# Kernel tuning notes

Hardware: AMD Instinct MI355X
Metric: run time of the kernel (lower is better)

Reference implementation:

```python
import jax, jax.numpy as jnp
import numpy as np

N, LT, LV, D, H = 4, 1024, 1024, 1024, 16
HD = D // H
EPS = 1e-12


def layernorm(x, w, b):
    u = x.mean(-1, keepdims=True)
    s = ((x - u) ** 2).mean(-1, keepdims=True)
    return w * (x - u) / jnp.sqrt(s + EPS) + b


def attention(q_in, k_in, v_in, mask, qw, qb, kw, kb, vw, vb):
    # mask: (N, Lq_or_1, Lk) float in {0,1}; torch Linear is x @ W.T + b
    def heads(x, w, b):
        y = x @ w.T + b
        return y.reshape(y.shape[0], y.shape[1], H, HD).transpose(0, 2, 1, 3)  # (N,H,L,hd)
    q, k, v = heads(q_in, qw, qb), heads(k_in, kw, kb), heads(v_in, vw, vb)
    scores = jnp.einsum('bhqd,bhkd->bhqk', q, k) / np.sqrt(HD).astype(np.float32)
    scores = scores + (1.0 - mask[:, None]) * (-10000.0)
    probs = jax.nn.softmax(scores, axis=-1)  # dropout is identity in eval
    ctx = jnp.einsum('bhqk,bhkd->bhqd', probs, v)
    return ctx.transpose(0, 2, 1, 3).reshape(q_in.shape[0], q_in.shape[1], D)


def setup_inputs() -> dict:
    key = jax.random.key(0)
    ks = jax.random.split(key, 16)
    inp = {
        'dec_hidden_states': jax.random.normal(ks[0], (N, LT, D), jnp.float32),
        'enc_outputs': jax.random.normal(ks[1], (N, LV, D), jnp.float32),
        'dec_mask': jnp.ones((N, LT), jnp.float32),
        'enc_mask': jnp.ones((N, LV), jnp.float32),
    }
    wnames = ['sa_qw', 'sa_kw', 'sa_vw', 'ca_qw', 'ca_kw', 'ca_vw', 'out_w']
    for i, n in enumerate(wnames):
        inp[n] = jax.random.normal(ks[2 + i], (D, D), jnp.float32) * 0.02
    for n in ['sa_qb', 'sa_kb', 'sa_vb', 'ca_qb', 'ca_kb', 'ca_vb', 'out_b', 'n1_b', 'n2_b', 'out_ln_b']:
        inp[n] = jnp.zeros((D,), jnp.float32)
    for n in ['n1_w', 'n2_w', 'out_ln_w']:
        inp[n] = jnp.ones((D,), jnp.float32)
    return inp


def reference(dec_hidden_states, enc_outputs, dec_mask, enc_mask,
              sa_qw, sa_qb, sa_kw, sa_kb, sa_vw, sa_vb, n1_w, n1_b,
              ca_qw, ca_qb, ca_kw, ca_kb, ca_vw, ca_vb, n2_w, n2_b,
              out_w, out_b, out_ln_w, out_ln_b):
    Lt = dec_mask.shape[1]
    # diagonal_mask=True: causal tril combined with padding mask
    self_mask = dec_mask[:, None, :] * jnp.tril(jnp.ones((Lt, Lt), dec_mask.dtype))  # (N,Lt,Lt)
    a = attention(dec_hidden_states, dec_hidden_states, dec_hidden_states, self_mask,
                  sa_qw, sa_qb, sa_kw, sa_kb, sa_vw, sa_vb)
    a = layernorm(a + dec_hidden_states, n1_w, n1_b)
    c = attention(a, enc_outputs, enc_outputs, enc_mask[:, None, :],
                  ca_qw, ca_qb, ca_kw, ca_kb, ca_vw, ca_vb)
    c = layernorm(a + c, n2_w, n2_b)
    # BertOutput called as output(x, x): dense, residual, LN (dropout = identity)
    h = c @ out_w.T + out_b
    return layernorm(h + c, out_ln_w, out_ln_b)
```

## Files before the change

kernel.cpp:

```cpp
#include <hip/hip_runtime.h>
#include <cstdint>
#include <cstddef>

typedef __bf16 bf16x8 __attribute__((ext_vector_type(8)));
typedef float  floatx4 __attribute__((ext_vector_type(4)));
typedef unsigned short ushortx8 __attribute__((ext_vector_type(8)));
typedef unsigned short ushortx4 __attribute__((ext_vector_type(4)));

#define MFMA16(a, b, c) __builtin_amdgcn_mfma_f32_16x16x32_bf16((a), (b), (c), 0, 0, 0)

__device__ inline unsigned short f2bf(float f) {
    unsigned int u = __float_as_uint(f);
    unsigned int r = (u + 0x7fffu + ((u >> 16) & 1u)) >> 16;
    return (unsigned short)r;
}

struct Src2 { const float* p[2]; };
__global__ __launch_bounds__(256) void k_x2_to_bf16(Src2 s2, unsigned short* __restrict__ dst) {
    int i = blockIdx.x * 256 + threadIdx.x;
    const float* src = s2.p[i >> 19];
    int off = i & 524287;
    const float4* s = (const float4*)src + (size_t)off * 2;
    float4 x0 = s[0], x1 = s[1];
    ushortx8 o;
    o[0] = f2bf(x0.x); o[1] = f2bf(x0.y); o[2] = f2bf(x0.z); o[3] = f2bf(x0.w);
    o[4] = f2bf(x1.x); o[5] = f2bf(x1.y); o[6] = f2bf(x1.z); o[7] = f2bf(x1.w);
    *((ushortx8*)dst + i) = o;
}
struct Src7 { const float* p[7]; };
__global__ __launch_bounds__(256) void k_w7_to_bf16(Src7 s7, unsigned short* __restrict__ dst) {
    int i = blockIdx.x * 256 + threadIdx.x;
    const float* src = s7.p[i >> 17];
    int off = i & 131071;
    const float4* s = (const float4*)src + (size_t)off * 2;
    float4 x0 = s[0], x1 = s[1];
    ushortx8 o;
    o[0] = f2bf(x0.x); o[1] = f2bf(x0.y); o[2] = f2bf(x0.z); o[3] = f2bf(x0.w);
    o[4] = f2bf(x1.x); o[5] = f2bf(x1.y); o[6] = f2bf(x1.z); o[7] = f2bf(x1.w);
    *((ushortx8*)dst + i) = o;
}

template <int MODE>
__global__ __launch_bounds__(256) void k_gemm_bias(const unsigned short* __restrict__ A,
                                                   const unsigned short* __restrict__ A2,
                                                   const unsigned short* __restrict__ W,
                                                   const float* __restrict__ bias0,
                                                   const float* __restrict__ bias1,
                                                   const float* __restrict__ bias2,
                                                   void* __restrict__ d0,
                                                   void* __restrict__ d1,
                                                   void* __restrict__ d2,
                                                   int K) {
    __shared__ __align__(16) unsigned short As[128 * 64];
    __shared__ __align__(16) unsigned short Bs[128 * 64];
    const int tid = threadIdx.x;
    const int wave = tid >> 6, lane = tid & 63;
    const int quad = lane >> 4, l15 = lane & 15;
    const int wm = wave >> 1, wn = wave & 1;

    constexpr int NT = (MODE == 3) ? 8 : 24;
    int fid = blockIdx.y * 32 + blockIdx.x;
    int xcd = fid & 7, idx = fid >> 3;
    const int m0 = (xcd * 4 + idx / NT) * 128;
    const int n0 = (idx % NT) * 128;
    const int sect_blk = n0 >> 10;

    const unsigned short* Ause = (MODE == 4 && sect_blk != 0) ? A2 : A;

    const size_t rowbytes = (size_t)K * 2;
    const int idx0 = tid, idx1 = 256 + tid;
    const char* pA0 = (const char*)Ause + (size_t)(m0 + (idx0 >> 2)) * rowbytes + ((idx0 & 3) << 4);
    const char* pA1 = (const char*)Ause + (size_t)(m0 + (idx1 >> 2)) * rowbytes + ((idx1 & 3) << 4);
    const char* pB0 = (const char*)W + (size_t)(n0 + (idx0 >> 2)) * rowbytes + ((idx0 & 3) << 4);
    const char* pB1 = (const char*)W + (size_t)(n0 + (idx1 >> 2)) * rowbytes + ((idx1 & 3) << 4);

    int4 a0a = *(const int4*)pA0, a0b = *(const int4*)(pA0 + 64);
    int4 a1a = *(const int4*)pA1, a1b = *(const int4*)(pA1 + 64);
    int4 b0a = *(const int4*)pB0, b0b = *(const int4*)(pB0 + 64);
    int4 b1a = *(const int4*)pB1, b1b = *(const int4*)(pB1 + 64);

    floatx4 acc[4][4] = {};

    const int KT = K >> 6;
    for (int kt = 0; kt < KT; ++kt) {
        __syncthreads();
        ((int4*)As)[idx0] = a0a; ((int4*)As)[idx1] = a1a;
        ((int4*)As)[512 + idx0] = a0b; ((int4*)As)[512 + idx1] = a1b;
        ((int4*)Bs)[idx0] = b0a; ((int4*)Bs)[idx1] = b1a;
        ((int4*)Bs)[512 + idx0] = b0b; ((int4*)Bs)[512 + idx1] = b1b;
        __syncthreads();
        if (kt + 1 < KT) {
            pA0 += 128; pA1 += 128; pB0 += 128; pB1 += 128;
            a0a = *(const int4*)pA0; a0b = *(const int4*)(pA0 + 64);
            a1a = *(const int4*)pA1; a1b = *(const int4*)(pA1 + 64);
            b0a = *(const int4*)pB0; b0b = *(const int4*)(pB0 + 64);
            b1a = *(const int4*)pB1; b1b = *(const int4*)(pB1 + 64);
        }
        const char* Asb = (const char*)As;
        const char* Bsb = (const char*)Bs;
#pragma unroll
        for (int half = 0; half < 2; ++half) {
            const int hb = half * 8192;
            bf16x8 af[4], bfr[4];
#pragma unroll
            for (int r = 0; r < 4; ++r)
                af[r] = *(const bf16x8*)(Asb + hb + ((wm * 64 + r * 16 + l15) * 64 + quad * 16));
#pragma unroll
            for (int c = 0; c < 4; ++c)
                bfr[c] = *(const bf16x8*)(Bsb + hb + ((wn * 64 + c * 16 + l15) * 64 + quad * 16));
#pragma unroll
            for (int r = 0; r < 4; ++r)
#pragma unroll
                for (int c = 0; c < 4; ++c)
                    acc[r][c] = MFMA16(af[r], bfr[c], acc[r][c]);
        }
    }

#pragma unroll
    for (int c = 0; c < 4; ++c) {
        int col = n0 + wn * 64 + c * 16 + l15;
        int sect = col >> 10, cc = col & 1023;
        float bv;
        if (MODE == 3) bv = bias0[col];
        else bv = (sect == 0 ? bias0 : (sect == 1 ? bias1 : bias2))[cc];
        int h = cc >> 6, d = cc & 63;
#pragma unroll
        for (int r = 0; r < 4; ++r) {
            int mrow = m0 + wm * 64 + r * 16 + quad * 4;
#pragma unroll
            for (int i = 0; i < 4; ++i) {
                float v = acc[r][c][i] + bv;
                int row = mrow + i;
                if (MODE == 3) {
                    ((float*)d0)[(size_t)row * 1024 + col] = v;
                } else {
                    int b = row >> 10, l = row & 1023;
                    unsigned short* base = (unsigned short*)(sect == 0 ? d0 : (sect == 1 ? d1 : d2));
                    bool isV = (sect == 2);
                    size_t off;
                    if (isV) {
                        int kk = l & 31;
                        int kperm = ((kk & 15) << 1) | (kk >> 4);
                        off = (size_t)(b * 16 + h) * 65536 + (size_t)(l >> 5) * 2048 + d * 32 + kperm;
                    } else {
                        off = ((size_t)(b * 16 + h) * 1024 + l) * 64 + d;
                    }
                    base[off] = f2bf(v);
                }
            }
        }
    }
}

__global__ __launch_bounds__(256, 4) void k_flash_attn(const unsigned short* __restrict__ Qp,
                                                       const unsigned short* __restrict__ Kp,
                                                       const unsigned short* __restrict__ Vp,
                                                       const float* __restrict__ mask,
                                                       float* __restrict__ ctx,
                                                       int causal) {
    const int L = 1024, D = 1024;
    const float SC = 0.18033688011112042f;
    int f = blockIdx.x;
    int g = f >> 7;
    int q = (f >> 3) & 15;
    int bh = (f & 7) + (g << 3);
    int qt = (q + 2 * g) & 15;
    int h = bh & 15, b = bh >> 4;
    int tid = threadIdx.x;
    int wave = tid >> 6, lane = tid & 63, quad = lane >> 4, l15 = lane & 15;
    int qbase = qt * 64 + wave * 16;

    __shared__ __align__(16) unsigned short Ks[4096];
    __shared__ __align__(16) unsigned short Vs[5120];
    __shared__ float penf[1024];
    __shared__ __align__(16) unsigned short Plds[4 * 1280];

    {
        float4 mv = ((const float4*)(mask + b * L))[tid];
        float4 pv;
        pv.x = (1.0f - mv.x) * -14426.950408889634f;
        pv.y = (1.0f - mv.y) * -14426.950408889634f;
        pv.z = (1.0f - mv.z) * -14426.950408889634f;
        pv.w = (1.0f - mv.w) * -14426.950408889634f;
        ((float4*)penf)[tid] = pv;
    }

    const unsigned short* Qh = Qp + ((size_t)(b * 16 + h) * 1024 + qbase) * 64;
    bf16x8 qf0 = *(const bf16x8*)(Qh + l15 * 64 + quad * 8);
    bf16x8 qf1 = *(const bf16x8*)(Qh + l15 * 64 + 32 + quad * 8);

    const char* Kh = (const char*)(Kp + (size_t)(b * 16 + h) * 65536);
    const char* Vh = (const char*)(Vp + (size_t)(b * 16 + h) * 65536);

    int ktiles = causal ? (qt + 1) : 16;

    char* Ksb = (char*)Ks;
    char* Vsb = (char*)Vs;
    int krow = tid >> 3, kblk = tid & 7;
    int kd0 = krow * 128 + ((kblk ^ (krow & 7)) << 4);
    int kd1 = kd0 + 32 * 128;
    int vd0 = (tid >> 2) * 80 + ((tid & 3) << 4);
    int vd1 = vd0 + 5120;

    int karA[4], karB[4];
#pragma unroll
    for (int r = 0; r < 4; ++r) {
        int row = r * 16 + l15;
        karA[r] = row * 128 + ((quad ^ (l15 & 7)) << 4);
        karB[r] = row * 128 + (((quad | 4) ^ (l15 & 7)) << 4);
    }
    int var_[8];
#pragma unroll
    for (int s = 0; s < 2; ++s)
#pragma unroll
        for (int fi = 0; fi < 4; ++fi)
            var_[s * 4 + fi] = s * 5120 + (fi * 16 + l15) * 80 + (quad << 4);

    floatx4 O[4] = {};
    float lsum[4] = {};
    unsigned short* pw = &Plds[wave * 1280];
    unsigned int* pw32 = (unsigned int*)pw;

    int4 ka0 = *(const int4*)(Kh + tid * 16);
    int4 ka1 = *(const int4*)(Kh + 4096 + tid * 16);
    int4 va0 = *(const int4*)(Vh + tid * 16);
    int4 va1 = *(const int4*)(Vh + 4096 + tid * 16);

    for (int kt = 0; kt < ktiles; ++kt) {
        *(int4*)(Ksb + kd0) = ka0;
        *(int4*)(Ksb + kd1) = ka1;
        *(int4*)(Vsb + vd0) = va0;
        *(int4*)(Vsb + vd1) = va1;
        __syncthreads();
        if (kt + 1 < ktiles) {
            const char* Kg = Kh + (size_t)(kt + 1) * 8192;
            const char* Vg = Vh + (size_t)(kt + 1) * 8192;
            ka0 = *(const int4*)(Kg + tid * 16);
            ka1 = *(const int4*)(Kg + 4096 + tid * 16);
            va0 = *(const int4*)(Vg + tid * 16);
            va1 = *(const int4*)(Vg + 4096 + tid * 16);
        }
        int k0 = kt * 64;

        bf16x8 kA[4], kB[4];
#pragma unroll
        for (int r = 0; r < 4; ++r) {
            kA[r] = *(const bf16x8*)(Ksb + karA[r]);
            kB[r] = *(const bf16x8*)(Ksb + karB[r]);
        }
        bf16x8 vv[8];
#pragma unroll
        for (int s = 0; s < 8; ++s) vv[s] = *(const bf16x8*)(Vsb + var_[s]);
        float pr0 = penf[k0 + l15];
        float pr1 = penf[k0 + 16 + l15];
        float pr2 = penf[k0 + 32 + l15];
        float pr3 = penf[k0 + 48 + l15];

        bool boundary = causal && (k0 + 63 > qbase);

        floatx4 S0 = {}, S1 = {}, S2 = {}, S3 = {};
        S0 = MFMA16(qf0, kA[0], S0); S0 = MFMA16(qf1, kB[0], S0);
        S1 = MFMA16(qf0, kA[1], S1); S1 = MFMA16(qf1, kB[1], S1);
        S2 = MFMA16(qf0, kA[2], S2); S2 = MFMA16(qf1, kB[2], S2);
        S3 = MFMA16(qf0, kA[3], S3); S3 = MFMA16(qf1, kB[3], S3);

        int qrow = qbase + quad * 4;
#pragma unroll
        for (int i = 0; i < 4; ++i) {
            float x0 = fmaf(S0[i], SC, pr0);
            float x1 = fmaf(S1[i], SC, pr1);
            float x2 = fmaf(S2[i], SC, pr2);
            float x3 = fmaf(S3[i], SC, pr3);
            if (boundary) {
                int qq = qrow + i;
                x0 = ((k0 + l15) <= qq) ? x0 : -50000.0f;
                x1 = ((k0 + 16 + l15) <= qq) ? x1 : -50000.0f;
                x2 = ((k0 + 32 + l15) <= qq) ? x2 : -50000.0f;
                x3 = ((k0 + 48 + l15) <= qq) ? x3 : -50000.0f;
            }
            float p0 = __builtin_amdgcn_exp2f(x0);
            float p1 = __builtin_amdgcn_exp2f(x1);
            float p2 = __builtin_amdgcn_exp2f(x2);
            float p3 = __builtin_amdgcn_exp2f(x3);
            lsum[i] += (p0 + p1) + (p2 + p3);
            unsigned r0 = __float_as_uint(p0) + 0x8000u;
            unsigned r1 = __float_as_uint(p1) + 0x8000u;
            unsigned r2 = __float_as_uint(p2) + 0x8000u;
            unsigned r3 = __float_as_uint(p3) + 0x8000u;
            unsigned plo = __builtin_amdgcn_perm(r1, r0, 0x07060302u);
            unsigned phi = __builtin_amdgcn_perm(r3, r2, 0x07060302u);
            int ro = (quad * 4 + i) * 20;
            pw32[ro + l15] = plo;
            pw32[320 + ro + l15] = phi;
        }
        bf16x8 pa_lo = *(const bf16x8*)(pw + l15 * 40 + quad * 8);
        bf16x8 pa_hi = *(const bf16x8*)(pw + 640 + l15 * 40 + quad * 8);
        O[0] = MFMA16(pa_lo, vv[0], O[0]);
        O[1] = MFMA16(pa_lo, vv[1], O[1]);
        O[2] = MFMA16(pa_lo, vv[2], O[2]);
        O[3] = MFMA16(pa_lo, vv[3], O[3]);
        O[0] = MFMA16(pa_hi, vv[4], O[0]);
        O[1] = MFMA16(pa_hi, vv[5], O[1]);
        O[2] = MFMA16(pa_hi, vv[6], O[2]);
        O[3] = MFMA16(pa_hi, vv[7], O[3]);
        __syncthreads();
    }

#pragma unroll
    for (int i = 0; i < 4; ++i) {
        float l = lsum[i];
        l += __shfl_xor(l, 1);
        l += __shfl_xor(l, 2);
        l += __shfl_xor(l, 4);
        l += __shfl_xor(l, 8);
        float inv = 1.0f / l;
        int qi = qbase + quad * 4 + i;
        float* op = ctx + ((size_t)(b * L + qi)) * D + h * 64;
#pragma unroll
        for (int fi = 0; fi < 4; ++fi) op[fi * 16 + l15] = O[fi][i] * inv;
    }
}

__global__ __launch_bounds__(256) void k_add_ln(const float* __restrict__ X,
                                                const float* __restrict__ Y,
                                                const float* __restrict__ w,
                                                const float* __restrict__ bvec,
                                                float* __restrict__ outf,
                                                unsigned short* __restrict__ outbf) {
    int row = blockIdx.x;
    int tid = threadIdx.x;
    float4 x = *((const float4*)(X + (size_t)row * 1024) + tid);
    float4 y = *((const float4*)(Y + (size_t)row * 1024) + tid);
    float v0 = x.x + y.x, v1 = x.y + y.y, v2 = x.z + y.z, v3 = x.w + y.w;
    float s = v0 + v1 + v2 + v3;
    float s2 = v0 * v0 + v1 * v1 + v2 * v2 + v3 * v3;
#pragma unroll
    for (int off = 32; off > 0; off >>= 1) {
        s += __shfl_xor(s, off);
        s2 += __shfl_xor(s2, off);
    }
    __shared__ float red[8];
    int wave = tid >> 6, lane = tid & 63;
    if (lane == 0) { red[wave] = s; red[4 + wave] = s2; }
    __syncthreads();
    s = red[0] + red[1] + red[2] + red[3];
    s2 = red[4] + red[5] + red[6] + red[7];
    float u = s * (1.0f / 1024.0f);
    float var = s2 * (1.0f / 1024.0f) - u * u;
    float r = 1.0f / sqrtf(fmaxf(var, 0.0f) + 1e-12f);
    float4 wv = *((const float4*)w + tid);
    float4 bv = *((const float4*)bvec + tid);
    float o0 = wv.x * (v0 - u) * r + bv.x;
    float o1 = wv.y * (v1 - u) * r + bv.y;
    float o2 = wv.z * (v2 - u) * r + bv.z;
    float o3 = wv.w * (v3 - u) * r + bv.w;
    float4 o = {o0, o1, o2, o3};
    *((float4*)(outf + (size_t)row * 1024) + tid) = o;
    if (outbf) {
        ushortx4 ob;
        ob[0] = f2bf(o0); ob[1] = f2bf(o1); ob[2] = f2bf(o2); ob[3] = f2bf(o3);
        *((ushortx4*)outbf + (size_t)row * 256 + tid) = ob;
    }
}

extern "C" void kernel_launch(void* const* d_in, const int* in_sizes, int n_in,
                              void* d_out, int out_size, void* d_ws, size_t ws_size,
                              hipStream_t stream) {
    (void)in_sizes; (void)n_in; (void)out_size; (void)ws_size;
    const float* dec = (const float*)d_in[0];
    const float* enc = (const float*)d_in[1];
    const float* dec_mask = (const float*)d_in[2];
    const float* enc_mask = (const float*)d_in[3];
    const float* b_saq = (const float*)d_in[11];
    const float* b_sak = (const float*)d_in[12];
    const float* b_sav = (const float*)d_in[13];
    const float* b_caq = (const float*)d_in[14];
    const float* b_cak = (const float*)d_in[15];
    const float* b_cav = (const float*)d_in[16];
    const float* b_out = (const float*)d_in[17];
    const float* n1_b = (const float*)d_in[18];
    const float* n2_b = (const float*)d_in[19];
    const float* oln_b = (const float*)d_in[20];
    const float* n1_w = (const float*)d_in[21];
    const float* n2_w = (const float*)d_in[22];
    const float* oln_w = (const float*)d_in[23];

    char* ws = (char*)d_ws;
    const size_t MB2 = 2097152;
    const size_t ACT_BF = 8388608;
    const size_t ACT_F32 = 16777216;
    unsigned short* Wbf[7];
    for (int i = 0; i < 7; ++i) Wbf[i] = (unsigned short*)(ws + i * MB2);
    size_t off = 7 * MB2;
    unsigned short* Xbf = (unsigned short*)(ws + off); off += ACT_BF;
    unsigned short* Ebf = (unsigned short*)(ws + off); off += ACT_BF;
    unsigned short* Abf = (unsigned short*)(ws + off); off += ACT_BF;
    unsigned short* Cbf = (unsigned short*)(ws + off); off += ACT_BF;
    unsigned short* Qp = (unsigned short*)(ws + off); off += ACT_BF;
    unsigned short* Kp = (unsigned short*)(ws + off); off += ACT_BF;
    unsigned short* Vp = (unsigned short*)(ws + off); off += ACT_BF;
    float* ctx = (float*)(ws + off); off += ACT_F32;
    float* a_f32 = (float*)(ws + off); off += ACT_F32;
    float* c_f32 = (float*)(ws + off); off += ACT_F32;
    float* h_f32 = ctx;
    float* outp = (float*)d_out;

    dim3 blk(256);
    dim3 attn_grid(1024);

    Src2 s2; s2.p[0] = dec; s2.p[1] = enc;
    k_x2_to_bf16<<<dim3(4096), blk, 0, stream>>>(s2, Xbf);
    Src7 s7;
    for (int i = 0; i < 7; ++i) s7.p[i] = (const float*)d_in[4 + i];
    k_w7_to_bf16<<<dim3(3584), blk, 0, stream>>>(s7, Wbf[0]);

    k_gemm_bias<0><<<dim3(32, 24), blk, 0, stream>>>(Xbf, Xbf, Wbf[0], b_saq, b_sak, b_sav,
                                                     Qp, Kp, Vp, 1024);
    k_flash_attn<<<attn_grid, blk, 0, stream>>>(Qp, Kp, Vp, dec_mask, ctx, 1);
    k_add_ln<<<dim3(4096), blk, 0, stream>>>(ctx, dec, n1_w, n1_b, a_f32, Abf);

    k_gemm_bias<4><<<dim3(32, 24), blk, 0, stream>>>(Abf, Ebf, Wbf[3], b_caq, b_cak, b_cav,
                                                     Qp, Kp, Vp, 1024);
    k_flash_attn<<<attn_grid, blk, 0, stream>>>(Qp, Kp, Vp, enc_mask, ctx, 0);
    k_add_ln<<<dim3(4096), blk, 0, stream>>>(a_f32, ctx, n2_w, n2_b, c_f32, Cbf);

    k_gemm_bias<3><<<dim3(32, 8), blk, 0, stream>>>(Cbf, Cbf, Wbf[6], b_out, b_out, b_out,
                                                    h_f32, nullptr, nullptr, 1024);
    k_add_ln<<<dim3(4096), blk, 0, stream>>>(h_f32, c_f32, oln_w, oln_b, outp, (unsigned short*)nullptr);
}
```

Baseline: 331.8 us.

## Compute transposed scores, pass P via permlane swaps, double-buffer K/V LDS

The flash attention kernel now computes S^T (K as A operand, Q as B), so each lane holds scores for a single query. The probability fragment is rearranged for the PV MFMA with v_permlane32/16_swap instead of a round trip through an LDS scratch buffer. The V layout permutation is dropped to match. K/V tiles are double-buffered in LDS, so the next tile's stores happen after compute and only one barrier is needed per iteration. The causal boundary check is limited to the last tile and the row sum reduction is simplified. The cost is twice the K/V LDS footprint, which may affect occupancy.

```diff
diff --git a/kernel.cpp b/kernel.cpp
--- a/kernel.cpp
+++ b/kernel.cpp
@@ -140,8 +140,7 @@
                     size_t off;
                     if (isV) {
                         int kk = l & 31;
-                        int kperm = ((kk & 15) << 1) | (kk >> 4);
-                        off = (size_t)(b * 16 + h) * 65536 + (size_t)(l >> 5) * 2048 + d * 32 + kperm;
+                        off = (size_t)(b * 16 + h) * 65536 + (size_t)(l >> 5) * 2048 + d * 32 + kk;
                     } else {
                         off = ((size_t)(b * 16 + h) * 1024 + l) * 64 + d;
                     }
@@ -162,18 +161,17 @@
     const float SC = 0.18033688011112042f;
     int f = blockIdx.x;
     int g = f >> 7;
-    int q = (f >> 3) & 15;
+    int qsel = (f >> 3) & 15;
     int bh = (f & 7) + (g << 3);
-    int qt = (q + 2 * g) & 15;
+    int qt = (qsel + 2 * g) & 15;
     int h = bh & 15, b = bh >> 4;
     int tid = threadIdx.x;
     int wave = tid >> 6, lane = tid & 63, quad = lane >> 4, l15 = lane & 15;
     int qbase = qt * 64 + wave * 16;
 
-    __shared__ __align__(16) unsigned short Ks[4096];
-    __shared__ __align__(16) unsigned short Vs[5120];
+    __shared__ __align__(16) unsigned short Ks[2 * 4096];
+    __shared__ __align__(16) unsigned short Vs[2 * 5120];
     __shared__ float penf[1024];
-    __shared__ __align__(16) unsigned short Plds[4 * 1280];
 
     {
         float4 mv = ((const float4*)(mask + b * L))[tid];
@@ -194,11 +192,9 @@
 
     int ktiles = causal ? (qt + 1) : 16;
 
-    char* Ksb = (char*)Ks;
-    char* Vsb = (char*)Vs;
     int krow = tid >> 3, kblk = tid & 7;
     int kd0 = krow * 128 + ((kblk ^ (krow & 7)) << 4);
-    int kd1 = kd0 + 32 * 128;
+    int kd1 = kd0 + 4096;
     int vd0 = (tid >> 2) * 80 + ((tid & 3) << 4);
     int vd1 = vd0 + 5120;
 
@@ -217,22 +213,39 @@
             var_[s * 4 + fi] = s * 5120 + (fi * 16 + l15) * 80 + (quad << 4);
 
     floatx4 O[4] = {};
-    float lsum[4] = {};
-    unsigned short* pw = &Plds[wave * 1280];
-    unsigned int* pw32 = (unsigned int*)pw;
+    float lsum = 0.0f;
 
     int4 ka0 = *(const int4*)(Kh + tid * 16);
     int4 ka1 = *(const int4*)(Kh + 4096 + tid * 16);
     int4 va0 = *(const int4*)(Vh + tid * 16);
     int4 va1 = *(const int4*)(Vh + 4096 + tid * 16);
+    {
+        char* Kw = (char*)Ks;
+        char* Vw = (char*)Vs;
+        *(int4*)(Kw + kd0) = ka0;
+        *(int4*)(Kw + kd1) = ka1;
+        *(int4*)(Vw + vd0) = va0;
+        *(int4*)(Vw + vd1) = va1;
+    }
+    __syncthreads();
 
     for (int kt = 0; kt < ktiles; ++kt) {
-        *(int4*)(Ksb + kd0) = ka0;
-        *(int4*)(Ksb + kd1) = ka1;
-        *(int4*)(Vsb + vd0) = va0;
-        *(int4*)(Vsb + vd1) = va1;
-        __syncthreads();
-        if (kt + 1 < ktiles) {
+        const char* Ksb = (const char*)Ks + (size_t)(kt & 1) * 8192;
+        const char* Vsb = (const char*)Vs + (size_t)(kt & 1) * 10240;
+        int k0 = kt * 64;
+        bool last = (kt + 1 >= ktiles);
+
+        bf16x8 kA[4], kB[4];
+#pragma unroll
+        for (int r = 0; r < 4; ++r) {
+            kA[r] = *(const bf16x8*)(Ksb + karA[r]);
+            kB[r] = *(const bf16x8*)(Ksb + karB[r]);
+        }
+        bf16x8 vv[8];
+#pragma unroll
+        for (int s = 0; s < 8; ++s) vv[s] = *(const bf16x8*)(Vsb + var_[s]);
+
+        if (!last) {
             const char* Kg = Kh + (size_t)(kt + 1) * 8192;
             const char* Vg = Vh + (size_t)(kt + 1) * 8192;
             ka0 = *(const int4*)(Kg + tid * 16);
@@ -240,80 +253,79 @@
             va0 = *(const int4*)(Vg + tid * 16);
             va1 = *(const int4*)(Vg + 4096 + tid * 16);
         }
-        int k0 = kt * 64;
-
-        bf16x8 kA[4], kB[4];
-#pragma unroll
-        for (int r = 0; r < 4; ++r) {
-            kA[r] = *(const bf16x8*)(Ksb + karA[r]);
-            kB[r] = *(const bf16x8*)(Ksb + karB[r]);
-        }
-        bf16x8 vv[8];
-#pragma unroll
-        for (int s = 0; s < 8; ++s) vv[s] = *(const bf16x8*)(Vsb + var_[s]);
-        float pr0 = penf[k0 + l15];
-        float pr1 = penf[k0 + 16 + l15];
-        float pr2 = penf[k0 + 32 + l15];
-        float pr3 = penf[k0 + 48 + l15];
-
-        bool boundary = causal && (k0 + 63 > qbase);
-
-        floatx4 S0 = {}, S1 = {}, S2 = {}, S3 = {};
-        S0 = MFMA16(qf0, kA[0], S0); S0 = MFMA16(qf1, kB[0], S0);
-        S1 = MFMA16(qf0, kA[1], S1); S1 = MFMA16(qf1, kB[1], S1);
-        S2 = MFMA16(qf0, kA[2], S2); S2 = MFMA16(qf1, kB[2], S2);
-        S3 = MFMA16(qf0, kA[3], S3); S3 = MFMA16(qf1, kB[3], S3);
-
-        int qrow = qbase + quad * 4;
-#pragma unroll
-        for (int i = 0; i < 4; ++i) {
-            float x0 = fmaf(S0[i], SC, pr0);
-            float x1 = fmaf(S1[i], SC, pr1);
-            float x2 = fmaf(S2[i], SC, pr2);
-            float x3 = fmaf(S3[i], SC, pr3);
-            if (boundary) {
-                int qq = qrow + i;
-                x0 = ((k0 + l15) <= qq) ? x0 : -50000.0f;
-                x1 = ((k0 + 16 + l15) <= qq) ? x1 : -50000.0f;
-                x2 = ((k0 + 32 + l15) <= qq) ? x2 : -50000.0f;
-                x3 = ((k0 + 48 + l15) <= qq) ? x3 : -50000.0f;
+
+        floatx4 T[4] = {};
+        T[0] = MFMA16(kA[0], qf0, T[0]); T[0] = MFMA16(kB[0], qf1, T[0]);
+        T[1] = MFMA16(kA[1], qf0, T[1]); T[1] = MFMA16(kB[1], qf1, T[1]);
+        T[2] = MFMA16(kA[2], qf0, T[2]); T[2] = MFMA16(kB[2], qf1, T[2]);
+        T[3] = MFMA16(kA[3], qf0, T[3]); T[3] = MFMA16(kB[3], qf1, T[3]);
+
+        bool boundary = causal && (kt == ktiles - 1);
+        int qv = qbase + l15;
+
+        unsigned w_[4][2];
+#pragma unroll
+        for (int s = 0; s < 4; ++s) {
+            floatx4 pr = *(const floatx4*)(penf + k0 + 16 * s + quad * 4);
+            unsigned rr[4];
+#pragma unroll
+            for (int i = 0; i < 4; ++i) {
+                float x = fmaf(T[s][i], SC, pr[i]);
+                if (boundary) {
+                    int key = k0 + 16 * s + quad * 4 + i;
+                    x = (key <= qv) ? x : -50000.0f;
+                }
+                float p = __builtin_amdgcn_exp2f(x);
+                lsum += p;
+                rr[i] = __float_as_uint(p) + 0x8000u;
             }
-            float p0 = __builtin_amdgcn_exp2f(x0);
-            float p1 = __builtin_amdgcn_exp2f(x1);
-            float p2 = __builtin_amdgcn_exp2f(x2);
-            float p3 = __builtin_amdgcn_exp2f(x3);
-            lsum[i] += (p0 + p1) + (p2 + p3);
-            unsigned r0 = __float_as_uint(p0) + 0x8000u;
-            unsigned r1 = __float_as_uint(p1) + 0x8000u;
-            unsigned r2 = __float_as_uint(p2) + 0x8000u;
-            unsigned r3 = __float_as_uint(p3) + 0x8000u;
-            unsigned plo = __builtin_amdgcn_perm(r1, r0, 0x07060302u);
-            unsigned phi = __builtin_amdgcn_perm(r3, r2, 0x07060302u);
-            int ro = (quad * 4 + i) * 20;
-            pw32[ro + l15] = plo;
-            pw32[320 + ro + l15] = phi;
-        }
-        bf16x8 pa_lo = *(const bf16x8*)(pw + l15 * 40 + quad * 8);
-        bf16x8 pa_hi = *(const bf16x8*)(pw + 640 + l15 * 40 + quad * 8);
-        O[0] = MFMA16(pa_lo, vv[0], O[0]);
-        O[1] = MFMA16(pa_lo, vv[1], O[1]);
-        O[2] = MFMA16(pa_lo, vv[2], O[2]);
-        O[3] = MFMA16(pa_lo, vv[3], O[3]);
-        O[0] = MFMA16(pa_hi, vv[4], O[0]);
-        O[1] = MFMA16(pa_hi, vv[5], O[1]);
-        O[2] = MFMA16(pa_hi, vv[6], O[2]);
-        O[3] = MFMA16(pa_hi, vv[7], O[3]);
+            w_[s][0] = __builtin_amdgcn_perm(rr[1], rr[0], 0x07060302u);
+            w_[s][1] = __builtin_amdgcn_perm(rr[3], rr[2], 0x07060302u);
+        }
+
+        unsigned a00 = w_[0][0], a10 = w_[1][0];
+        unsigned a01 = w_[0][1], a11 = w_[1][1];
+        unsigned a20 = w_[2][0], a30 = w_[3][0];
+        unsigned a21 = w_[2][1], a31 = w_[3][1];
+        asm("v_permlane32_swap_b32 %0, %1" : "+v"(a00), "+v"(a10));
+        asm("v_permlane32_swap_b32 %0, %1" : "+v"(a01), "+v"(a11));
+        asm("v_permlane32_swap_b32 %0, %1" : "+v"(a20), "+v"(a30));
+        asm("v_permlane32_swap_b32 %0, %1" : "+v"(a21), "+v"(a31));
+        asm("v_permlane16_swap_b32 %0, %1" : "+v"(a00), "+v"(a10));
+        asm("v_permlane16_swap_b32 %0, %1" : "+v"(a01), "+v"(a11));
+        asm("v_permlane16_swap_b32 %0, %1" : "+v"(a20), "+v"(a30));
+        asm("v_permlane16_swap_b32 %0, %1" : "+v"(a21), "+v"(a31));
+        union PU { unsigned u[4]; bf16x8 v; };
+        PU pl, ph;
+        pl.u[0] = a00; pl.u[1] = a01; pl.u[2] = a10; pl.u[3] = a11;
+        ph.u[0] = a20; ph.u[1] = a21; ph.u[2] = a30; ph.u[3] = a31;
+
+        O[0] = MFMA16(pl.v, vv[0], O[0]);
+        O[1] = MFMA16(pl.v, vv[1], O[1]);
+        O[2] = MFMA16(pl.v, vv[2], O[2]);
+        O[3] = MFMA16(pl.v, vv[3], O[3]);
+        O[0] = MFMA16(ph.v, vv[4], O[0]);
+        O[1] = MFMA16(ph.v, vv[5], O[1]);
+        O[2] = MFMA16(ph.v, vv[6], O[2]);
+        O[3] = MFMA16(ph.v, vv[7], O[3]);
+
+        if (!last) {
+            char* Kw = (char*)Ks + (size_t)((kt + 1) & 1) * 8192;
+            char* Vw = (char*)Vs + (size_t)((kt + 1) & 1) * 10240;
+            *(int4*)(Kw + kd0) = ka0;
+            *(int4*)(Kw + kd1) = ka1;
+            *(int4*)(Vw + vd0) = va0;
+            *(int4*)(Vw + vd1) = va1;
+        }
         __syncthreads();
     }
 
+    lsum += __shfl_xor(lsum, 16);
+    lsum += __shfl_xor(lsum, 32);
 #pragma unroll
     for (int i = 0; i < 4; ++i) {
-        float l = lsum[i];
-        l += __shfl_xor(l, 1);
-        l += __shfl_xor(l, 2);
-        l += __shfl_xor(l, 4);
-        l += __shfl_xor(l, 8);
-        float inv = 1.0f / l;
+        float lt = __shfl(lsum, quad * 4 + i);
+        float inv = 1.0f / lt;
         int qi = qbase + quad * 4 + i;
         float* op = ctx + ((size_t)(b * L + qi)) * D + h * 64;
 #pragma unroll
```

Result: no change. 329.4 us (-0.7%).
